# Optimization experiments

Hardware: AMD Instinct MI355X
Metric: run time of the kernel (lower is better)

## Reference

```python
import jax, jax.numpy as jnp
import numpy as np
from jax import lax

L = 2048      # sentence length
V = 50000     # vocab size
E = 512       # embedding dim
HD = 512      # per-direction hidden (hidden_dim // 2)
H = 1024      # hidden_dim
T = 48        # tagset size
START, STOP = 46, 47
NEG = -10000.0


def setup_inputs() -> dict:
    key = jax.random.key(0)
    ks = iter(jax.random.split(key, 40))
    def n(shape, s=0.1):
        return jax.random.normal(next(ks), shape, dtype=jnp.float32) * s
    inp = {"sentence": jax.random.randint(next(ks), (L,), 0, V, dtype=jnp.int32)}
    inp["embedding"] = n((V, E), 1.0)
    for l, din in ((0, E), (1, H)):
        for d in ("", "r"):
            inp[f"w_ih_l{l}{d}"] = n((4 * HD, din))
            inp[f"w_hh_l{l}{d}"] = n((4 * HD, HD))
            inp[f"b_ih_l{l}{d}"] = n((4 * HD,))
            inp[f"b_hh_l{l}{d}"] = n((4 * HD,))
    inp["h0"] = n((4, HD), 1.0)
    inp["c0"] = n((4, HD), 1.0)
    inp["W_tag"] = n((T, H))
    inp["b_tag"] = n((T,))
    tr = n((T, T), 1.0)
    inp["transitions"] = tr.at[START, :].set(NEG).at[:, STOP].set(NEG)
    return inp


def _lstm_dir(x, w_ih, w_hh, b_ih, b_hh, h, c, reverse):
    # PyTorch LSTM cell, gates ordered (i, f, g, o). x: [L, Din]
    pre = x @ w_ih.T + (b_ih + b_hh)  # [L, 4*HD]
    def step(carry, p):
        h, c = carry
        g = p + h @ w_hh.T
        i, f, gg, o = jnp.split(g, 4)
        i, f, o = jax.nn.sigmoid(i), jax.nn.sigmoid(f), jax.nn.sigmoid(o)
        c = f * c + i * jnp.tanh(gg)
        h = o * jnp.tanh(c)
        return (h, c), h
    _, hs = lax.scan(step, (h, c), pre, reverse=reverse)
    return hs  # [L, HD], time-aligned with input


def _viterbi(feats, transitions):
    # max-plus recurrence over the tagset, vectorized per timestep
    init = jnp.full((T,), NEG, dtype=feats.dtype).at[START].set(0.0)
    def step(fv, feat):
        scores = fv[None, :] + transitions  # [next_tag, prev_tag]
        bp = jnp.argmax(scores, axis=1)
        return jnp.max(scores, axis=1) + feat, bp
    fv, bps = lax.scan(step, init, feats)  # bps: [L, T]
    terminal = fv + transitions[STOP]
    best = jnp.argmax(terminal)
    score = terminal[best]
    def back(tag, bp):
        prev = bp[tag]
        return prev, prev
    _, ys = lax.scan(back, best, bps, reverse=True)
    # ys[0] == START (dropped); path is tags for t = 0..L-1
    path = jnp.concatenate([ys[1:], best[None]])
    return score, path


def reference(sentence, embedding,
              w_ih_l0, w_hh_l0, b_ih_l0, b_hh_l0,
              w_ih_l0r, w_hh_l0r, b_ih_l0r, b_hh_l0r,
              w_ih_l1, w_hh_l1, b_ih_l1, b_hh_l1,
              w_ih_l1r, w_hh_l1r, b_ih_l1r, b_hh_l1r,
              h0, c0, W_tag, b_tag, transitions):
    embeds = embedding[sentence]  # [L, E]
    l0 = jnp.concatenate([
        _lstm_dir(embeds, w_ih_l0, w_hh_l0, b_ih_l0, b_hh_l0, h0[0], c0[0], False),
        _lstm_dir(embeds, w_ih_l0r, w_hh_l0r, b_ih_l0r, b_hh_l0r, h0[1], c0[1], True),
    ], axis=-1)  # [L, H]
    l1 = jnp.concatenate([
        _lstm_dir(l0, w_ih_l1, w_hh_l1, b_ih_l1, b_hh_l1, h0[2], c0[2], False),
        _lstm_dir(l0, w_ih_l1r, w_hh_l1r, b_ih_l1r, b_hh_l1r, h0[3], c0[3], True),
    ], axis=-1)  # [L, H]
    feats = l1 @ W_tag.T + b_tag  # [L, T]
    score, path = _viterbi(feats, transitions)
    return score, path
```

## Files before the change

kernel.cpp:

```cpp
#include <hip/hip_runtime.h>
#include <hip/hip_bf16.h>

#define L_SEQ 2048
#define HDIM 512
#define NGATE4 2048
#define TAGS 48
#define START_TAG 46
#define STOP_TAG 47
#define NWG 32
#define JPW 16

typedef float f32x4 __attribute__((ext_vector_type(4)));

#define BM 64
#define BN 64
#define BK 32
#define LDT 68

__global__ __launch_bounds__(256, 2)
void gemm_abt(const float* __restrict__ A, const float* __restrict__ B,
              const float* __restrict__ bias1, const float* __restrict__ bias2,
              float* __restrict__ C, int M, int N, int K,
              const int* __restrict__ gather)
{
  __shared__ float As[BK][LDT];
  __shared__ float Bs[BK][LDT];
  const int tid = threadIdx.x;
  const int m0 = blockIdx.x * BM;
  const int n0 = blockIdx.y * BN;
  const int tm = tid >> 4, tn = tid & 15;
  const int lr = tid >> 2, lk = (tid & 3) * 8;

  float acc[4][4];
#pragma unroll
  for (int i = 0; i < 4; ++i)
#pragma unroll
    for (int c = 0; c < 4; ++c) acc[i][c] = 0.f;

  const int am = m0 + lr;
  const float* arow = gather ? (A + (size_t)gather[am] * (size_t)K)
                             : (A + (size_t)am * (size_t)K);
  const int bn = n0 + lr;
  const float* brow = B + (size_t)bn * (size_t)K;
  const bool bok = (bn < N);

  for (int kt = 0; kt < K; kt += BK) {
    const float4 a0 = *(const float4*)(arow + kt + lk);
    const float4 a1 = *(const float4*)(arow + kt + lk + 4);
    float4 b0 = make_float4(0.f, 0.f, 0.f, 0.f);
    float4 b1 = make_float4(0.f, 0.f, 0.f, 0.f);
    if (bok) {
      b0 = *(const float4*)(brow + kt + lk);
      b1 = *(const float4*)(brow + kt + lk + 4);
    }
    As[lk + 0][lr] = a0.x; As[lk + 1][lr] = a0.y; As[lk + 2][lr] = a0.z; As[lk + 3][lr] = a0.w;
    As[lk + 4][lr] = a1.x; As[lk + 5][lr] = a1.y; As[lk + 6][lr] = a1.z; As[lk + 7][lr] = a1.w;
    Bs[lk + 0][lr] = b0.x; Bs[lk + 1][lr] = b0.y; Bs[lk + 2][lr] = b0.z; Bs[lk + 3][lr] = b0.w;
    Bs[lk + 4][lr] = b1.x; Bs[lk + 5][lr] = b1.y; Bs[lk + 6][lr] = b1.z; Bs[lk + 7][lr] = b1.w;
    __syncthreads();
#pragma unroll
    for (int kk = 0; kk < BK; ++kk) {
      const float4 av = *(const float4*)&As[kk][tm * 4];
      const float4 bv = *(const float4*)&Bs[kk][tn * 4];
      const float aa[4] = {av.x, av.y, av.z, av.w};
      const float bb[4] = {bv.x, bv.y, bv.z, bv.w};
#pragma unroll
      for (int i = 0; i < 4; ++i)
#pragma unroll
        for (int c = 0; c < 4; ++c)
          acc[i][c] += aa[i] * bb[c];
    }
    __syncthreads();
  }

  float bsum[4];
#pragma unroll
  for (int c = 0; c < 4; ++c) {
    const int n = n0 + tn * 4 + c;
    float bb = 0.f;
    if (n < N) { bb = bias1[n]; if (bias2) bb += bias2[n]; }
    bsum[c] = bb;
  }
#pragma unroll
  for (int i = 0; i < 4; ++i) {
    const int m = m0 + tm * 4 + i;
#pragma unroll
    for (int c = 0; c < 4; ++c) {
      const int n = n0 + tn * 4 + c;
      if (n < N) C[(size_t)m * N + n] = acc[i][c] + bsum[c];
    }
  }
}

__global__ __launch_bounds__(512, 1)
void lstm_layer(const float* __restrict__ pre_f, const float* __restrict__ pre_r,
                const float* __restrict__ whh_f, const float* __restrict__ whh_r,
                const float* __restrict__ h0, const float* __restrict__ c0,
                int hcrow_base,
                float* __restrict__ hs_out,
                unsigned int* __restrict__ xch)
{
  const int dir = blockIdx.x & 1;
  const int wg  = blockIdx.x >> 1;
  const float* pre = dir ? pre_r : pre_f;
  const float* whh = dir ? whh_r : whh_f;
  const int tid = threadIdx.x;
  const int lane = tid & 63;
  const int wave = tid >> 6;
  const int q = lane & 15;
  const int g = lane >> 4;
  const int j0 = wg * JPW + wave * 2;
  const int hc = (hcrow_base + dir) * HDIM;
  const unsigned base = (unsigned)((hcrow_base >> 1) * 2048);

  __shared__ f32x4 wlds[8][2][8][64];
  __shared__ float h_lds[HDIM];

#pragma unroll
  for (int jj = 0; jj < 2; ++jj) {
    const float* wr = whh + (size_t)(g * HDIM + j0 + jj) * HDIM + 32 * q;
#pragma unroll
    for (int i = 0; i < 8; ++i)
      wlds[wave][jj][i][lane] = *(const f32x4*)(wr + 4 * ((i + q) & 7));
  }
  h_lds[tid] = h0[hc + tid];
  float cA = 0.f, cB = 0.f;
  if (lane == 0) { cA = c0[hc + j0]; cB = c0[hc + j0 + 1]; }
  __syncthreads();

  float pa = 0.f, pb = 0.f;
  if (q == 0) {
    const int t0 = dir ? (L_SEQ - 1) : 0;
    const float* pr = pre + (size_t)t0 * NGATE4 + g * HDIM + j0;
    pa = pr[0]; pb = pr[1];
  }

  for (int s = 0; s < L_SEQ; ++s) {
    const int t = dir ? (L_SEQ - 1 - s) : s;
    float pna = 0.f, pnb = 0.f;
    if (q == 0 && (s + 1 < L_SEQ)) {
      const int tnx = dir ? (L_SEQ - 2 - s) : (s + 1);
      const float* pr = pre + (size_t)tnx * NGATE4 + g * HDIM + j0;
      pna = pr[0]; pnb = pr[1];
    }

    f32x4 accA = {0.f, 0.f, 0.f, 0.f};
    f32x4 accB = {0.f, 0.f, 0.f, 0.f};
#pragma unroll
    for (int i = 0; i < 8; ++i) {
      const f32x4 hv = *(const f32x4*)&h_lds[32 * q + 4 * ((i + q) & 7)];
      accA += wlds[wave][0][i][lane] * hv;
      accB += wlds[wave][1][i][lane] * hv;
    }
    float aA = accA.x + accA.y + accA.z + accA.w;
    float aB = accB.x + accB.y + accB.z + accB.w;
#pragma unroll
    for (int m = 1; m < 16; m <<= 1) {
      aA += __shfl_xor(aA, m, 64);
      aB += __shfl_xor(aB, m, 64);
    }
    aA += pa; aB += pb;

    const float fA = __shfl(aA, 16, 64), gA = __shfl(aA, 32, 64), oA = __shfl(aA, 48, 64);
    const float fB = __shfl(aB, 16, 64), gB = __shfl(aB, 32, 64), oB = __shfl(aB, 48, 64);

    if (lane == 0) {
      const unsigned tag = base + (unsigned)s + 1u;
      const size_t ob = (size_t)t * 1024 + dir * HDIM + j0;
      unsigned* xp = xch + ((s + 1) & 1) * 1024 + dir * HDIM + j0;
      {
        const float si = 1.f / (1.f + __expf(-aA));
        const float sf = 1.f / (1.f + __expf(-fA));
        const float tg = 1.f - 2.f / (__expf(2.f * gA) + 1.f);
        const float so = 1.f / (1.f + __expf(-oA));
        cA = sf * cA + si * tg;
        const float h = so * (1.f - 2.f / (__expf(2.f * cA) + 1.f));
        hs_out[ob] = h;
        unsigned u = __float_as_uint(h);
        u = (u + 0x7FFFu + ((u >> 16) & 1u)) & 0xFFFF0000u;
        __hip_atomic_store(xp, u | tag, __ATOMIC_RELAXED, __HIP_MEMORY_SCOPE_AGENT);
      }
      {
        const float si = 1.f / (1.f + __expf(-aB));
        const float sf = 1.f / (1.f + __expf(-fB));
        const float tg = 1.f - 2.f / (__expf(2.f * gB) + 1.f);
        const float so = 1.f / (1.f + __expf(-oB));
        cB = sf * cB + si * tg;
        const float h = so * (1.f - 2.f / (__expf(2.f * cB) + 1.f));
        hs_out[ob + 1] = h;
        unsigned u = __float_as_uint(h);
        u = (u + 0x7FFFu + ((u >> 16) & 1u)) & 0xFFFF0000u;
        __hip_atomic_store(xp + 1, u | tag, __ATOMIC_RELAXED, __HIP_MEMORY_SCOPE_AGENT);
      }
    }
    pa = pna; pb = pnb;

    if (s == L_SEQ - 1) break;

    __syncthreads();
    {
      const unsigned expect = base + (unsigned)s + 1u;
      const unsigned* wp = xch + ((s + 1) & 1) * 1024 + dir * HDIM + tid;
      unsigned v;
      do {
        v = __hip_atomic_load(wp, __ATOMIC_RELAXED, __HIP_MEMORY_SCOPE_AGENT);
      } while ((v & 0xFFFFu) != expect);
      h_lds[tid] = __uint_as_float(v & 0xFFFF0000u);
    }
    __syncthreads();
  }
}

__global__ __launch_bounds__(192, 1)
void viterbi_kernel(const float* __restrict__ feats,
                    const float* __restrict__ trans,
                    int* __restrict__ bp,
                    float* __restrict__ out)
{
  __shared__ float fv[TAGS];
  __shared__ float fvn[TAGS];
  const int tid = threadIdx.x;
  const int lane = tid & 63;
  const int wave = tid >> 6;
  const int q = lane & 3;
  const int j = wave * 16 + (lane >> 2);

  float trr[12];
#pragma unroll
  for (int kk = 0; kk < 12; ++kk) trr[kk] = trans[j * TAGS + q * 12 + kk];

  if (tid < TAGS) fv[tid] = (tid == START_TAG) ? 0.f : -10000.f;
  __syncthreads();

  for (int t = 0; t < L_SEQ; ++t) {
    const float ft = feats[t * TAGS + j];
    float best = -3.0e38f;
    int bi = 0;
#pragma unroll
    for (int kk = 0; kk < 12; ++kk) {
      const int k = q * 12 + kk;
      const float sc = fv[k] + trr[kk];
      if (sc > best) { best = sc; bi = k; }
    }
#pragma unroll
    for (int m = 1; m < 4; m <<= 1) {
      const float ov = __shfl_xor(best, m, 64);
      const int oi = __shfl_xor(bi, m, 64);
      if (ov > best || (ov == best && oi < bi)) { best = ov; bi = oi; }
    }
    __syncthreads();
    if (q == 0) {
      bp[t * TAGS + j] = bi;
      fv[j] = best + ft;
    }
    __syncthreads();
  }

  if (tid < TAGS) fvn[tid] = fv[tid] + trans[STOP_TAG * TAGS + tid];
  __syncthreads();
  if (tid == 0) {
    float best = -3.0e38f;
    int bi = 0;
    for (int k = 0; k < TAGS; ++k) {
      const float v = fvn[k];
      if (v > best) { best = v; bi = k; }
    }
    out[0] = best;
    int cur = bi;
    out[1 + (L_SEQ - 1)] = (float)cur;
    for (int t = L_SEQ - 2; t >= 0; --t) {
      cur = bp[(t + 1) * TAGS + cur];
      out[1 + t] = (float)cur;
    }
  }
}

extern "C" void kernel_launch(void* const* d_in, const int* in_sizes, int n_in,
                              void* d_out, int out_size, void* d_ws, size_t ws_size,
                              hipStream_t stream)
{
  const int*   sentence  = (const int*)  d_in[0];
  const float* embedding = (const float*)d_in[1];
  const float* w_ih_l0   = (const float*)d_in[2];
  const float* w_hh_l0   = (const float*)d_in[3];
  const float* b_ih_l0   = (const float*)d_in[4];
  const float* b_hh_l0   = (const float*)d_in[5];
  const float* w_ih_l0r  = (const float*)d_in[6];
  const float* w_hh_l0r  = (const float*)d_in[7];
  const float* b_ih_l0r  = (const float*)d_in[8];
  const float* b_hh_l0r  = (const float*)d_in[9];
  const float* w_ih_l1   = (const float*)d_in[10];
  const float* w_hh_l1   = (const float*)d_in[11];
  const float* b_ih_l1   = (const float*)d_in[12];
  const float* b_hh_l1   = (const float*)d_in[13];
  const float* w_ih_l1r  = (const float*)d_in[14];
  const float* w_hh_l1r  = (const float*)d_in[15];
  const float* b_ih_l1r  = (const float*)d_in[16];
  const float* b_hh_l1r  = (const float*)d_in[17];
  const float* h0        = (const float*)d_in[18];
  const float* c0        = (const float*)d_in[19];
  const float* W_tag     = (const float*)d_in[20];
  const float* b_tag     = (const float*)d_in[21];
  const float* trans     = (const float*)d_in[22];

  float* ws    = (float*)d_ws;
  float* pre_f = ws;
  float* pre_r = pre_f + (size_t)L_SEQ * NGATE4;
  float* l0out = pre_r + (size_t)L_SEQ * NGATE4;
  float* l1out = l0out + (size_t)L_SEQ * 1024;
  float* feats = l1out + (size_t)L_SEQ * 1024;
  unsigned int* xch = (unsigned int*)(feats + (size_t)L_SEQ * TAGS);
  int*   bp    = (int*)(xch + 2048);

  (void)hipMemsetAsync(xch, 0, 2048 * sizeof(unsigned int), stream);

  dim3 blk(256);
  dim3 gfull(L_SEQ / BM, NGATE4 / BN);
  gemm_abt<<<gfull, blk, 0, stream>>>(embedding, w_ih_l0, b_ih_l0, b_hh_l0,
                                      pre_f, L_SEQ, NGATE4, 512, sentence);
  gemm_abt<<<gfull, blk, 0, stream>>>(embedding, w_ih_l0r, b_ih_l0r, b_hh_l0r,
                                      pre_r, L_SEQ, NGATE4, 512, sentence);
  lstm_layer<<<2 * NWG, 512, 0, stream>>>(pre_f, pre_r, w_hh_l0, w_hh_l0r,
                                          h0, c0, 0, l0out, xch);
  gemm_abt<<<gfull, blk, 0, stream>>>(l0out, w_ih_l1, b_ih_l1, b_hh_l1,
                                      pre_f, L_SEQ, NGATE4, 1024, nullptr);
  gemm_abt<<<gfull, blk, 0, stream>>>(l0out, w_ih_l1r, b_ih_l1r, b_hh_l1r,
                                      pre_r, L_SEQ, NGATE4, 1024, nullptr);
  lstm_layer<<<2 * NWG, 512, 0, stream>>>(pre_f, pre_r, w_hh_l1, w_hh_l1r,
                                          h0, c0, 2, l1out, xch);
  dim3 gfeat(L_SEQ / BM, 1);
  gemm_abt<<<gfeat, blk, 0, stream>>>(l1out, W_tag, b_tag, nullptr,
                                      feats, L_SEQ, TAGS, 1024, nullptr);
  viterbi_kernel<<<1, 192, 0, stream>>>(feats, trans, bp, (float*)d_out);
}
```

Measured before the change: 15.07 ms.

## Halve LSTM workgroups, store recurrent weights as bf16 in LDS, exchange full fp32 h

The recurrent LSTM kernel now runs 16 workgroups per direction with 1024 threads each instead of 32 with 512, so fewer workgroups take part in the per-step global spin-wait exchange. To fit twice the hidden units per workgroup in LDS, W_hh is stored as packed bf16 and widened to fp32 at use. The h exchange moves from a 32-bit bf16-plus-tag word to a 64-bit word holding fp32 h and the tag. The trade is extra unpacking ALU work and bf16 weight rounding, against cheaper cross-workgroup synchronisation and a more exact h value.

```diff
diff --git a/kernel.cpp b/kernel.cpp
--- a/kernel.cpp
+++ b/kernel.cpp
@@ -7,8 +7,8 @@
 #define TAGS 48
 #define START_TAG 46
 #define STOP_TAG 47
-#define NWG 32
-#define JPW 16
+#define NWG 16
+#define JPW 32
 
 typedef float f32x4 __attribute__((ext_vector_type(4)));
 
@@ -92,13 +92,20 @@
   }
 }
 
-__global__ __launch_bounds__(512, 1)
+__device__ __forceinline__ unsigned bf16pk(float a, float b) {
+  unsigned ua = __float_as_uint(a), ub = __float_as_uint(b);
+  ua = ua + 0x7FFFu + ((ua >> 16) & 1u);
+  ub = ub + 0x7FFFu + ((ub >> 16) & 1u);
+  return (ua >> 16) | (ub & 0xFFFF0000u);
+}
+
+__global__ __launch_bounds__(1024, 1)
 void lstm_layer(const float* __restrict__ pre_f, const float* __restrict__ pre_r,
                 const float* __restrict__ whh_f, const float* __restrict__ whh_r,
                 const float* __restrict__ h0, const float* __restrict__ c0,
                 int hcrow_base,
                 float* __restrict__ hs_out,
-                unsigned int* __restrict__ xch)
+                unsigned long long* __restrict__ xch)
 {
   const int dir = blockIdx.x & 1;
   const int wg  = blockIdx.x >> 1;
@@ -113,17 +120,22 @@
   const int hc = (hcrow_base + dir) * HDIM;
   const unsigned base = (unsigned)((hcrow_base >> 1) * 2048);
 
-  __shared__ f32x4 wlds[8][2][8][64];
+  __shared__ uint2 wlds[16][2][8][64];
   __shared__ float h_lds[HDIM];
 
 #pragma unroll
   for (int jj = 0; jj < 2; ++jj) {
     const float* wr = whh + (size_t)(g * HDIM + j0 + jj) * HDIM + 32 * q;
 #pragma unroll
-    for (int i = 0; i < 8; ++i)
-      wlds[wave][jj][i][lane] = *(const f32x4*)(wr + 4 * ((i + q) & 7));
-  }
-  h_lds[tid] = h0[hc + tid];
+    for (int i = 0; i < 8; ++i) {
+      const float4 v = *(const float4*)(wr + 4 * ((i + q) & 7));
+      uint2 pk;
+      pk.x = bf16pk(v.x, v.y);
+      pk.y = bf16pk(v.z, v.w);
+      wlds[wave][jj][i][lane] = pk;
+    }
+  }
+  if (tid < HDIM) h_lds[tid] = h0[hc + tid];
   float cA = 0.f, cB = 0.f;
   if (lane == 0) { cA = c0[hc + j0]; cB = c0[hc + j0 + 1]; }
   __syncthreads();
@@ -149,8 +161,16 @@
 #pragma unroll
     for (int i = 0; i < 8; ++i) {
       const f32x4 hv = *(const f32x4*)&h_lds[32 * q + 4 * ((i + q) & 7)];
-      accA += wlds[wave][0][i][lane] * hv;
-      accB += wlds[wave][1][i][lane] * hv;
+      const uint2 wA = wlds[wave][0][i][lane];
+      const uint2 wB = wlds[wave][1][i][lane];
+      accA.x += __uint_as_float(wA.x << 16)         * hv.x;
+      accA.y += __uint_as_float(wA.x & 0xFFFF0000u) * hv.y;
+      accA.z += __uint_as_float(wA.y << 16)         * hv.z;
+      accA.w += __uint_as_float(wA.y & 0xFFFF0000u) * hv.w;
+      accB.x += __uint_as_float(wB.x << 16)         * hv.x;
+      accB.y += __uint_as_float(wB.x & 0xFFFF0000u) * hv.y;
+      accB.z += __uint_as_float(wB.y << 16)         * hv.z;
+      accB.w += __uint_as_float(wB.y & 0xFFFF0000u) * hv.w;
     }
     float aA = accA.x + accA.y + accA.z + accA.w;
     float aB = accB.x + accB.y + accB.z + accB.w;
@@ -165,9 +185,9 @@
     const float fB = __shfl(aB, 16, 64), gB = __shfl(aB, 32, 64), oB = __shfl(aB, 48, 64);
 
     if (lane == 0) {
-      const unsigned tag = base + (unsigned)s + 1u;
+      const unsigned long long tag = (unsigned long long)(base + (unsigned)s + 1u);
       const size_t ob = (size_t)t * 1024 + dir * HDIM + j0;
-      unsigned* xp = xch + ((s + 1) & 1) * 1024 + dir * HDIM + j0;
+      unsigned long long* xp = xch + ((s + 1) & 1) * 1024 + dir * HDIM + j0;
       {
         const float si = 1.f / (1.f + __expf(-aA));
         const float sf = 1.f / (1.f + __expf(-fA));
@@ -176,9 +196,9 @@
         cA = sf * cA + si * tg;
         const float h = so * (1.f - 2.f / (__expf(2.f * cA) + 1.f));
         hs_out[ob] = h;
-        unsigned u = __float_as_uint(h);
-        u = (u + 0x7FFFu + ((u >> 16) & 1u)) & 0xFFFF0000u;
-        __hip_atomic_store(xp, u | tag, __ATOMIC_RELAXED, __HIP_MEMORY_SCOPE_AGENT);
+        const unsigned long long w =
+            ((unsigned long long)__float_as_uint(h) << 32) | tag;
+        __hip_atomic_store(xp, w, __ATOMIC_RELAXED, __HIP_MEMORY_SCOPE_AGENT);
       }
       {
         const float si = 1.f / (1.f + __expf(-aB));
@@ -188,9 +208,9 @@
         cB = sf * cB + si * tg;
         const float h = so * (1.f - 2.f / (__expf(2.f * cB) + 1.f));
         hs_out[ob + 1] = h;
-        unsigned u = __float_as_uint(h);
-        u = (u + 0x7FFFu + ((u >> 16) & 1u)) & 0xFFFF0000u;
-        __hip_atomic_store(xp + 1, u | tag, __ATOMIC_RELAXED, __HIP_MEMORY_SCOPE_AGENT);
+        const unsigned long long w =
+            ((unsigned long long)__float_as_uint(h) << 32) | tag;
+        __hip_atomic_store(xp + 1, w, __ATOMIC_RELAXED, __HIP_MEMORY_SCOPE_AGENT);
       }
     }
     pa = pna; pb = pnb;
@@ -198,14 +218,14 @@
     if (s == L_SEQ - 1) break;
 
     __syncthreads();
-    {
+    if (tid < HDIM) {
       const unsigned expect = base + (unsigned)s + 1u;
-      const unsigned* wp = xch + ((s + 1) & 1) * 1024 + dir * HDIM + tid;
-      unsigned v;
+      const unsigned long long* wp = xch + ((s + 1) & 1) * 1024 + dir * HDIM + tid;
+      unsigned long long v;
       do {
         v = __hip_atomic_load(wp, __ATOMIC_RELAXED, __HIP_MEMORY_SCOPE_AGENT);
-      } while ((v & 0xFFFFu) != expect);
-      h_lds[tid] = __uint_as_float(v & 0xFFFF0000u);
+      } while ((unsigned)v != expect);
+      h_lds[tid] = __uint_as_float((unsigned)(v >> 32));
     }
     __syncthreads();
   }
@@ -309,10 +329,11 @@
   float* l0out = pre_r + (size_t)L_SEQ * NGATE4;
   float* l1out = l0out + (size_t)L_SEQ * 1024;
   float* feats = l1out + (size_t)L_SEQ * 1024;
-  unsigned int* xch = (unsigned int*)(feats + (size_t)L_SEQ * TAGS);
+  unsigned long long* xch =
+      (unsigned long long*)(feats + (size_t)L_SEQ * TAGS);
   int*   bp    = (int*)(xch + 2048);
 
-  (void)hipMemsetAsync(xch, 0, 2048 * sizeof(unsigned int), stream);
+  (void)hipMemsetAsync(xch, 0, 2048 * sizeof(unsigned long long), stream);
 
   dim3 blk(256);
   dim3 gfull(L_SEQ / BM, NGATE4 / BN);
@@ -320,14 +341,14 @@
                                       pre_f, L_SEQ, NGATE4, 512, sentence);
   gemm_abt<<<gfull, blk, 0, stream>>>(embedding, w_ih_l0r, b_ih_l0r, b_hh_l0r,
                                       pre_r, L_SEQ, NGATE4, 512, sentence);
-  lstm_layer<<<2 * NWG, 512, 0, stream>>>(pre_f, pre_r, w_hh_l0, w_hh_l0r,
-                                          h0, c0, 0, l0out, xch);
+  lstm_layer<<<2 * NWG, 1024, 0, stream>>>(pre_f, pre_r, w_hh_l0, w_hh_l0r,
+                                           h0, c0, 0, l0out, xch);
   gemm_abt<<<gfull, blk, 0, stream>>>(l0out, w_ih_l1, b_ih_l1, b_hh_l1,
                                       pre_f, L_SEQ, NGATE4, 1024, nullptr);
   gemm_abt<<<gfull, blk, 0, stream>>>(l0out, w_ih_l1r, b_ih_l1r, b_hh_l1r,
                                       pre_r, L_SEQ, NGATE4, 1024, nullptr);
-  lstm_layer<<<2 * NWG, 512, 0, stream>>>(pre_f, pre_r, w_hh_l1, w_hh_l1r,
-                                          h0, c0, 2, l1out, xch);
+  lstm_layer<<<2 * NWG, 1024, 0, stream>>>(pre_f, pre_r, w_hh_l1, w_hh_l1r,
+                                           h0, c0, 2, l1out, xch);
   dim3 gfeat(L_SEQ / BM, 1);
   gemm_abt<<<gfeat, blk, 0, stream>>>(l1out, W_tag, b_tag, nullptr,
                                       feats, L_SEQ, TAGS, 1024, nullptr);
```

Result: slower. 16.86 ms (+11.9%).

## Exchange full-precision hidden state via 64-bit tagged words and spread LSTM workgroups across XCDs

Applied to the files above, without the earlier changes.

The per-step hidden-state exchange now packs the full fp32 h value and the step tag into one 64-bit atomic word instead of rounding h to bf16 and sharing a 32-bit word with a 16-bit tag. The LSTM launch grows to 256 blocks, and only one in every four pairs does work, so the 64 active workgroups land with a stride of 8 in block index. This is presumably meant to put them on separate XCDs/CUs and cut L2 or CU contention during the spin-wait exchange. It restores precision in the recurrence, but it doubles the exchange traffic, launches 192 idle blocks, and relies on an assumed mapping of blocks to XCDs.

```diff
diff --git a/kernel.cpp b/kernel.cpp
--- a/kernel.cpp
+++ b/kernel.cpp
@@ -98,10 +98,12 @@
                 const float* __restrict__ h0, const float* __restrict__ c0,
                 int hcrow_base,
                 float* __restrict__ hs_out,
-                unsigned int* __restrict__ xch)
+                unsigned long long* __restrict__ xch)
 {
-  const int dir = blockIdx.x & 1;
-  const int wg  = blockIdx.x >> 1;
+  const int sel = blockIdx.x & 7;
+  if (sel > 1) return;
+  const int dir = sel;
+  const int wg  = blockIdx.x >> 3;
   const float* pre = dir ? pre_r : pre_f;
   const float* whh = dir ? whh_r : whh_f;
   const int tid = threadIdx.x;
@@ -165,9 +167,9 @@
     const float fB = __shfl(aB, 16, 64), gB = __shfl(aB, 32, 64), oB = __shfl(aB, 48, 64);
 
     if (lane == 0) {
-      const unsigned tag = base + (unsigned)s + 1u;
+      const unsigned long long tag = (unsigned long long)(base + (unsigned)s + 1u);
       const size_t ob = (size_t)t * 1024 + dir * HDIM + j0;
-      unsigned* xp = xch + ((s + 1) & 1) * 1024 + dir * HDIM + j0;
+      unsigned long long* xp = xch + ((s + 1) & 1) * 1024 + dir * HDIM + j0;
       {
         const float si = 1.f / (1.f + __expf(-aA));
         const float sf = 1.f / (1.f + __expf(-fA));
@@ -176,9 +178,9 @@
         cA = sf * cA + si * tg;
         const float h = so * (1.f - 2.f / (__expf(2.f * cA) + 1.f));
         hs_out[ob] = h;
-        unsigned u = __float_as_uint(h);
-        u = (u + 0x7FFFu + ((u >> 16) & 1u)) & 0xFFFF0000u;
-        __hip_atomic_store(xp, u | tag, __ATOMIC_RELAXED, __HIP_MEMORY_SCOPE_AGENT);
+        const unsigned long long w =
+            ((unsigned long long)__float_as_uint(h) << 32) | tag;
+        __hip_atomic_store(xp, w, __ATOMIC_RELAXED, __HIP_MEMORY_SCOPE_AGENT);
       }
       {
         const float si = 1.f / (1.f + __expf(-aB));
@@ -188,9 +190,9 @@
         cB = sf * cB + si * tg;
         const float h = so * (1.f - 2.f / (__expf(2.f * cB) + 1.f));
         hs_out[ob + 1] = h;
-        unsigned u = __float_as_uint(h);
-        u = (u + 0x7FFFu + ((u >> 16) & 1u)) & 0xFFFF0000u;
-        __hip_atomic_store(xp + 1, u | tag, __ATOMIC_RELAXED, __HIP_MEMORY_SCOPE_AGENT);
+        const unsigned long long w =
+            ((unsigned long long)__float_as_uint(h) << 32) | tag;
+        __hip_atomic_store(xp + 1, w, __ATOMIC_RELAXED, __HIP_MEMORY_SCOPE_AGENT);
       }
     }
     pa = pna; pb = pnb;
@@ -200,12 +202,12 @@
     __syncthreads();
     {
       const unsigned expect = base + (unsigned)s + 1u;
-      const unsigned* wp = xch + ((s + 1) & 1) * 1024 + dir * HDIM + tid;
-      unsigned v;
+      const unsigned long long* wp = xch + ((s + 1) & 1) * 1024 + dir * HDIM + tid;
+      unsigned long long v;
       do {
         v = __hip_atomic_load(wp, __ATOMIC_RELAXED, __HIP_MEMORY_SCOPE_AGENT);
-      } while ((v & 0xFFFFu) != expect);
-      h_lds[tid] = __uint_as_float(v & 0xFFFF0000u);
+      } while ((unsigned)v != expect);
+      h_lds[tid] = __uint_as_float((unsigned)(v >> 32));
     }
     __syncthreads();
   }
@@ -309,10 +311,11 @@
   float* l0out = pre_r + (size_t)L_SEQ * NGATE4;
   float* l1out = l0out + (size_t)L_SEQ * 1024;
   float* feats = l1out + (size_t)L_SEQ * 1024;
-  unsigned int* xch = (unsigned int*)(feats + (size_t)L_SEQ * TAGS);
+  unsigned long long* xch =
+      (unsigned long long*)(feats + (size_t)L_SEQ * TAGS);
   int*   bp    = (int*)(xch + 2048);
 
-  (void)hipMemsetAsync(xch, 0, 2048 * sizeof(unsigned int), stream);
+  (void)hipMemsetAsync(xch, 0, 2048 * sizeof(unsigned long long), stream);
 
   dim3 blk(256);
   dim3 gfull(L_SEQ / BM, NGATE4 / BN);
@@ -320,14 +323,14 @@
                                       pre_f, L_SEQ, NGATE4, 512, sentence);
   gemm_abt<<<gfull, blk, 0, stream>>>(embedding, w_ih_l0r, b_ih_l0r, b_hh_l0r,
                                       pre_r, L_SEQ, NGATE4, 512, sentence);
-  lstm_layer<<<2 * NWG, 512, 0, stream>>>(pre_f, pre_r, w_hh_l0, w_hh_l0r,
-                                          h0, c0, 0, l0out, xch);
+  lstm_layer<<<256, 512, 0, stream>>>(pre_f, pre_r, w_hh_l0, w_hh_l0r,
+                                      h0, c0, 0, l0out, xch);
   gemm_abt<<<gfull, blk, 0, stream>>>(l0out, w_ih_l1, b_ih_l1, b_hh_l1,
                                       pre_f, L_SEQ, NGATE4, 1024, nullptr);
   gemm_abt<<<gfull, blk, 0, stream>>>(l0out, w_ih_l1r, b_ih_l1r, b_hh_l1r,
                                       pre_r, L_SEQ, NGATE4, 1024, nullptr);
-  lstm_layer<<<2 * NWG, 512, 0, stream>>>(pre_f, pre_r, w_hh_l1, w_hh_l1r,
-                                          h0, c0, 2, l1out, xch);
+  lstm_layer<<<256, 512, 0, stream>>>(pre_f, pre_r, w_hh_l1, w_hh_l1r,
+                                      h0, c0, 2, l1out, xch);
   dim3 gfeat(L_SEQ / BM, 1);
   gemm_abt<<<gfeat, blk, 0, stream>>>(l1out, W_tag, b_tag, nullptr,
                                       feats, L_SEQ, TAGS, 1024, nullptr);
```

Result: slower. 15.54 ms (+3.1%).
